# Performance work log

Hardware: AMD Instinct MI355X
Metric: run time of the kernel (lower is better)

## Reference

```python
import math
import jax, jax.numpy as jnp
import numpy as np

B_SZ, N_TOK, D_INNER, S_STATE = 4, 1024, 384, 16
DT_MAX = 0.15


def setup_inputs() -> dict:
    key = jax.random.key(0)
    ks = jax.random.split(key, 10)
    dt_init = math.log(math.exp(0.1) - 1.0)  # softplus^-1(0.1)
    x = jax.random.normal(ks[0], (B_SZ, N_TOK, D_INNER), dtype=jnp.float32)
    dt_self_W = jax.random.uniform(ks[1], (D_INNER, D_INNER), minval=-1e-4, maxval=1e-4)
    dt_self_b = jnp.full((D_INNER,), dt_init, dtype=jnp.float32)
    dt_diff_W = jax.random.uniform(ks[2], (D_INNER, D_INNER), minval=-1e-4, maxval=1e-4)
    dt_diff_b = jnp.full((D_INNER,), dt_init, dtype=jnp.float32)
    B_W = jax.random.normal(ks[3], (D_INNER, S_STATE)) / math.sqrt(D_INNER)
    C_real_W = jax.random.normal(ks[4], (D_INNER, S_STATE)) / math.sqrt(D_INNER)
    C_imag_W = jax.random.normal(ks[5], (D_INNER, S_STATE)) / math.sqrt(D_INNER)
    D_param = jnp.ones((D_INNER,), dtype=jnp.float32)
    A_log = jnp.broadcast_to(jnp.log(jnp.arange(1, S_STATE + 1, dtype=jnp.float32))[None, :], (D_INNER, S_STATE))
    lap = jnp.array([[0.0, 1.0, 0.0], [1.0, -4.0, 1.0], [0.0, 1.0, 0.0]], dtype=jnp.float32) * 0.1
    conv_w = jnp.broadcast_to(lap[None, None], (D_INNER, 1, 3, 3)) + 0.01 * jax.random.normal(ks[6], (D_INNER, 1, 3, 3))
    reaction_alpha = 0.01 * jax.random.normal(ks[7], (1, 1, D_INNER, 1))
    reaction_beta = 0.01 * jax.random.normal(ks[8], (1, 1, D_INNER, 1))
    return {
        'x': x, 'dt_self_W': dt_self_W, 'dt_self_b': dt_self_b,
        'dt_diff_W': dt_diff_W, 'dt_diff_b': dt_diff_b,
        'B_W': B_W, 'C_real_W': C_real_W, 'C_imag_W': C_imag_W,
        'D_param': D_param, 'A_log': A_log, 'conv_w': conv_w,
        'reaction_alpha': reaction_alpha, 'reaction_beta': reaction_beta,
        'K_steps': 2,
    }


def _laplacian(h, conv_w, H, W):
    # h: (B, N, D, S) -> depthwise 3x3 conv with replicate pad over the HxW grid
    B, N, D, S = h.shape
    hs = h.transpose(0, 3, 2, 1).reshape(B * S, D, H, W)
    hp = jnp.pad(hs, ((0, 0), (0, 0), (1, 1), (1, 1)), mode='edge')
    lap = jax.lax.conv_general_dilated(
        hp, conv_w, window_strides=(1, 1), padding='VALID',
        feature_group_count=D, dimension_numbers=('NCHW', 'OIHW', 'NCHW'))
    return lap.reshape(B, S, D, N).transpose(0, 3, 2, 1)


def reference(x, dt_self_W, dt_self_b, dt_diff_W, dt_diff_b, B_W, C_real_W,
              C_imag_W, D_param, A_log, conv_w, reaction_alpha, reaction_beta,
              K_steps):
    B, N, D = x.shape
    H = Wg = int(math.sqrt(N))
    A = -jax.nn.softplus(A_log)  # (D, S)
    delta_s = jnp.minimum(jax.nn.softplus(x @ dt_self_W.T + dt_self_b), DT_MAX)[..., None]
    delta_d = jnp.minimum(jax.nn.softplus(x @ dt_diff_W.T + dt_diff_b), DT_MAX)[..., None]
    B_mat = x @ B_W          # (B, N, S)
    C_real = x @ C_real_W    # (B, N, S)
    C_imag = x @ C_imag_W    # (B, N, S)
    mamba_input = jnp.einsum('bnd,bns->bnds', x, B_mat)
    h_real = mamba_input
    h_imag = jnp.zeros_like(h_real)
    dt = 1.0 / K_steps
    A_exp = A[None, None]  # (1,1,D,S)
    for _ in range(K_steps):
        f1_real = delta_s * (A_exp * h_real + mamba_input)
        f1_imag = delta_s * (A_exp * h_imag)
        lap_real = _laplacian(h_real, conv_w, H, Wg)
        lap_imag = _laplacian(h_imag, conv_w, H, Wg)
        f2_real = delta_d * -lap_imag
        f2_imag = delta_d * lap_real
        reaction_scale = reaction_alpha - reaction_beta * (h_real ** 2 + h_imag ** 2)
        h_real = h_real + dt * (f1_real + f2_real + h_real * reaction_scale)
        h_imag = h_imag + dt * (f1_imag + f2_imag + h_imag * reaction_scale)
    y = (jnp.einsum('bnds,bns->bnd', h_real, C_real)
         + jnp.einsum('bnds,bns->bnd', h_imag, C_imag)
         + x * D_param)
    return y
```

## Files before the change

### kernel.cpp

```cpp
#include <hip/hip_runtime.h>
#include <math.h>

#define B_SZ    4
#define N_TOKC  1024
#define D_INNER 384
#define S_STATE 16
#define DT_MAX_V 0.15f
#define PLANE   (B_SZ * N_TOKC)
#define DN      ((size_t)B_SZ * D_INNER * N_TOKC)

typedef __attribute__((ext_vector_type(8))) short bf16x8;
typedef __attribute__((ext_vector_type(4))) float f32x4;

__device__ __forceinline__ float softplusf(float z) {
    return fmaxf(z, 0.f) + log1pf(expf(-fabsf(z)));
}

__device__ __forceinline__ unsigned short f2bf(float f) {
    unsigned u = __float_as_uint(f);
    unsigned r = (u + 0x7FFFu + ((u >> 16) & 1u)) >> 16;
    return (unsigned short)r;
}

__device__ __forceinline__ unsigned packbf(float hr, float hi) {
    return (__float_as_uint(hr) & 0xFFFF0000u) | (__float_as_uint(hi) >> 16);
}

__device__ __forceinline__ size_t frag_off(int T, int kb, int q, int l16) {
    return ((size_t)((T * 12 + kb) * 4 + q)) * 128 + l16 * 8;
}

__device__ __forceinline__ bf16x8 pack8(const float* v) {
    bf16x8 o;
#pragma unroll
    for (int e = 0; e < 8; e++) o[e] = (short)f2bf(v[e]);
    return o;
}

__global__ __launch_bounds__(256) void k_prep(
    const float* __restrict__ x, const float* __restrict__ Ws, const float* __restrict__ Wd,
    const float* __restrict__ BW, const float* __restrict__ CrW, const float* __restrict__ CiW,
    float* __restrict__ x_t, unsigned short* __restrict__ xp,
    unsigned short* __restrict__ Wdtp, unsigned short* __restrict__ Wbcp)
{
    const int t = threadIdx.x;
    const int bx = blockIdx.x;
    if (bx < 1536) {
        __shared__ __align__(16) float tile[32][36];
        const int tok0 = (bx & 127) * 32;
        const int d0   = (bx >> 7) * 32;
        const int b = tok0 >> 10, n0 = tok0 & 1023;
        {
            const int r = t >> 3, c4 = (t & 7) * 4;
            const float4 v = *(const float4*)(x + (size_t)(tok0 + r) * D_INNER + d0 + c4);
            tile[r][c4 + 0] = v.x; tile[r][c4 + 1] = v.y;
            tile[r][c4 + 2] = v.z; tile[r][c4 + 3] = v.w;
        }
        __syncthreads();
        {
            const int dr = t >> 3, n4 = (t & 7) * 4;
            float4 o;
            o.x = tile[n4 + 0][dr]; o.y = tile[n4 + 1][dr];
            o.z = tile[n4 + 2][dr]; o.w = tile[n4 + 3][dr];
            *(float4*)(x_t + ((size_t)(b * D_INNER + d0 + dr)) * N_TOKC + n0 + n4) = o;
        }
        if (t < 128) {
            const int tt = t >> 6, q = (t >> 4) & 3, l16 = t & 15;
            const int row = tt * 16 + l16;
            float v[8];
#pragma unroll
            for (int e = 0; e < 8; e++) v[e] = tile[row][q * 8 + e];
            *(bf16x8*)(xp + frag_off((tok0 >> 4) + tt, d0 >> 5, q, l16)) = pack8(v);
        }
    } else if (bx < 1584) {
        const int vv = bx - 1536;
        const int mat = vv >= 24;
        const int dt16 = mat ? vv - 24 : vv;
        const float* W = mat ? Wd : Ws;
        unsigned short* dst = Wdtp + (size_t)mat * 147456;
#pragma unroll
        for (int it = 0; it < 3; it++) {
            const int item = t + it * 256;
            const int l16 = item & 15, q = (item >> 4) & 3, kb = item >> 6;
            const float* src = W + (size_t)(dt16 * 16 + l16) * D_INNER + kb * 32 + q * 8;
            float v[8];
            const float4 v0 = *(const float4*)(src);
            const float4 v1 = *(const float4*)(src + 4);
            v[0] = v0.x; v[1] = v0.y; v[2] = v0.z; v[3] = v0.w;
            v[4] = v1.x; v[5] = v1.y; v[6] = v1.z; v[7] = v1.w;
            *(bf16x8*)(dst + frag_off(dt16, kb, q, l16)) = pack8(v);
        }
    } else {
        const int m = bx - 1584;
        const float* W2 = (m == 0) ? BW : ((m == 1) ? CrW : CiW);
#pragma unroll
        for (int it = 0; it < 3; it++) {
            const int item = t + it * 256;
            const int l16 = item & 15, q = (item >> 4) & 3, kb = item >> 6;
            float v[8];
#pragma unroll
            for (int e = 0; e < 8; e++)
                v[e] = W2[(size_t)(kb * 32 + q * 8 + e) * S_STATE + l16];
            *(bf16x8*)(Wbcp + (size_t)m * 6144 + frag_off(0, kb, q, l16)) = pack8(v);
        }
    }
}

__global__ __launch_bounds__(256) void k_gemm(
    const unsigned short* __restrict__ xp, const unsigned short* __restrict__ Wdtp,
    const unsigned short* __restrict__ Wbcp,
    const float* __restrict__ bs, const float* __restrict__ bd,
    float* __restrict__ ds_t, float* __restrict__ dd_t,
    float* __restrict__ Bm_t, float* __restrict__ Cr_t, float* __restrict__ Ci_t)
{
    const int wave = threadIdx.x >> 6;
    const int lane = threadIdx.x & 63;
    const int quad = lane >> 4, l16 = lane & 15;

    if (blockIdx.x < 384) {
        const int dbase = (blockIdx.x >> 6) * 64;
        const int tbase = (blockIdx.x & 63) * 64;
        const int wd = (wave & 1) * 32;
        const int wt = (wave >> 1) * 32;
        const int dT0 = (dbase + wd) >> 4;
        const int tT0 = (tbase + wt) >> 4;

        f32x4 acc[2][2][2];
#pragma unroll
        for (int m = 0; m < 2; m++)
#pragma unroll
            for (int i = 0; i < 2; i++)
#pragma unroll
                for (int j = 0; j < 2; j++) acc[m][i][j] = (f32x4)0.f;

#pragma unroll
        for (int kb = 0; kb < 12; kb++) {
            bf16x8 a[2][2], b[2];
#pragma unroll
            for (int m = 0; m < 2; m++)
#pragma unroll
                for (int i = 0; i < 2; i++)
                    a[m][i] = *(const bf16x8*)(Wdtp + (size_t)m * 147456
                                               + frag_off(dT0 + i, kb, quad, l16));
#pragma unroll
            for (int j = 0; j < 2; j++)
                b[j] = *(const bf16x8*)(xp + frag_off(tT0 + j, kb, quad, l16));
#pragma unroll
            for (int m = 0; m < 2; m++)
#pragma unroll
                for (int i = 0; i < 2; i++)
#pragma unroll
                    for (int j = 0; j < 2; j++)
                        acc[m][i][j] = __builtin_amdgcn_mfma_f32_16x16x32_bf16(
                            a[m][i], b[j], acc[m][i][j], 0, 0, 0);
        }

#pragma unroll
        for (int m = 0; m < 2; m++) {
            const float* bias = (m == 0) ? bs : bd;
            float* out = (m == 0) ? ds_t : dd_t;
#pragma unroll
            for (int i = 0; i < 2; i++)
#pragma unroll
                for (int j = 0; j < 2; j++) {
                    const int tok = tbase + wt + j * 16 + l16;
                    const int bb = tok >> 10, n = tok & 1023;
#pragma unroll
                    for (int reg = 0; reg < 4; reg++) {
                        const int d = dbase + wd + i * 16 + quad * 4 + reg;
                        const float v = fminf(softplusf(acc[m][i][j][reg] + bias[d]), DT_MAX_V);
                        out[((size_t)(bb * D_INNER + d)) * N_TOKC + n] = v;
                    }
                }
        }
    } else {
        const int tT = (blockIdx.x - 384) * 4 + wave;
        f32x4 acc[3];
#pragma unroll
        for (int m = 0; m < 3; m++) acc[m] = (f32x4)0.f;

#pragma unroll
        for (int kb = 0; kb < 12; kb++) {
            const bf16x8 b = *(const bf16x8*)(xp + frag_off(tT, kb, quad, l16));
#pragma unroll
            for (int m = 0; m < 3; m++) {
                const bf16x8 a = *(const bf16x8*)(Wbcp + (size_t)m * 6144
                                                  + frag_off(0, kb, quad, l16));
                acc[m] = __builtin_amdgcn_mfma_f32_16x16x32_bf16(a, b, acc[m], 0, 0, 0);
            }
        }

        const int tok = tT * 16 + l16;
#pragma unroll
        for (int m = 0; m < 3; m++) {
            float* plane = (m == 0) ? Bm_t : ((m == 1) ? Cr_t : Ci_t);
#pragma unroll
            for (int reg = 0; reg < 4; reg++) {
                const int s = quad * 4 + reg;
                plane[(size_t)s * PLANE + tok] = acc[m][reg];
            }
        }
    }
}

__global__ __launch_bounds__(256) void k_ssm(
    const float* __restrict__ x_t, const float* __restrict__ conv_w, const float* __restrict__ A_log,
    const float* __restrict__ ralpha, const float* __restrict__ rbeta, const float* __restrict__ Dp,
    const float* __restrict__ ds_t, const float* __restrict__ dd_t,
    const float* __restrict__ Bm_t, const float* __restrict__ Cr_t, const float* __restrict__ Ci_t,
    float* __restrict__ y_part)
{
    const int sg = blockIdx.x;
    const int d  = blockIdx.y;
    const int b  = blockIdx.z;
    const int t  = threadIdx.x;
    const int c  = t & 31;
    const int g  = t >> 5;
    const int r0 = g * 4;

    __shared__ unsigned pl[4][34 * 34];

    float w[9];
#pragma unroll
    for (int i = 0; i < 9; i++) w[i] = conv_w[d * 9 + i];
    const float alpha = ralpha[d];
    const float beta  = rbeta[d];
    const float Dv    = Dp[d];
    float A[4];
#pragma unroll
    for (int s = 0; s < 4; s++) A[s] = -softplusf(A_log[d * S_STATE + sg * 4 + s]);

    const size_t base_dn = ((size_t)(b * D_INNER + d)) * N_TOKC;
    const size_t base_sn = (size_t)b * N_TOKC;

    float xv[4], dsv[4], ddv[4], Bmv[4][4];
    float hr[4][4], hi[4][4];
#pragma unroll
    for (int k = 0; k < 4; k++) {
        const int n = (r0 + k) * 32 + c;
        xv[k]  = x_t [base_dn + n];
        dsv[k] = ds_t[base_dn + n];
        ddv[k] = dd_t[base_dn + n];
#pragma unroll
        for (int s = 0; s < 4; s++) {
            Bmv[k][s] = Bm_t[(size_t)(sg * 4 + s) * PLANE + base_sn + n];
            hr[k][s]  = xv[k] * Bmv[k][s];
        }
    }

    const int wslot = (r0 + 1) * 34 + (c + 1);
    const int rbase = r0 * 34 + c;

#pragma unroll
    for (int s = 0; s < 4; s++) {
#pragma unroll
        for (int k = 0; k < 4; k++)
            pl[s][wslot + k * 34] = __float_as_uint(hr[k][s]);
        if (g == 0) pl[s][c + 1]           = __float_as_uint(hr[0][s]);
        if (g == 7) pl[s][33 * 34 + c + 1] = __float_as_uint(hr[3][s]);
        if (c == 0) {
#pragma unroll
            for (int k = 0; k < 4; k++) pl[s][(r0 + 1 + k) * 34] = __float_as_uint(hr[k][s]);
            if (g == 0) pl[s][0]       = __float_as_uint(hr[0][s]);
            if (g == 7) pl[s][33 * 34] = __float_as_uint(hr[3][s]);
        }
        if (c == 31) {
#pragma unroll
            for (int k = 0; k < 4; k++) pl[s][(r0 + 1 + k) * 34 + 33] = __float_as_uint(hr[k][s]);
            if (g == 0) pl[s][33]           = __float_as_uint(hr[0][s]);
            if (g == 7) pl[s][33 * 34 + 33] = __float_as_uint(hr[3][s]);
        }
    }
    __syncthreads();

    float lr0[4][4];
#pragma unroll
    for (int s = 0; s < 4; s++) {
        float fr[6][3];
#pragma unroll
        for (int rr = 0; rr < 6; rr++)
#pragma unroll
            for (int bb = 0; bb < 3; bb++)
                fr[rr][bb] = __uint_as_float(pl[s][rbase + rr * 34 + bb]);
#pragma unroll
        for (int k = 0; k < 4; k++) {
            float ar = 0.f;
#pragma unroll
            for (int a = 0; a < 3; a++)
#pragma unroll
                for (int bb = 0; bb < 3; bb++)
                    ar = fmaf(w[a * 3 + bb], fr[k + a][bb], ar);
            lr0[k][s] = ar;
        }
    }
    __syncthreads();

#pragma unroll
    for (int k = 0; k < 4; k++)
#pragma unroll
        for (int s = 0; s < 4; s++) {
            const float hrv = hr[k][s];
            const float u   = xv[k] * Bmv[k][s];
            const float f1r = dsv[k] * fmaf(A[s], hrv, u);
            const float rs  = fmaf(-beta, hrv * hrv, alpha);
            hr[k][s] = hrv + 0.5f * (f1r + hrv * rs);
            hi[k][s] = 0.5f * ddv[k] * lr0[k][s];
        }

#pragma unroll
    for (int s = 0; s < 4; s++) {
#pragma unroll
        for (int k = 0; k < 4; k++)
            pl[s][wslot + k * 34] = packbf(hr[k][s], hi[k][s]);
        if (g == 0) pl[s][c + 1]           = packbf(hr[0][s], hi[0][s]);
        if (g == 7) pl[s][33 * 34 + c + 1] = packbf(hr[3][s], hi[3][s]);
        if (c == 0) {
#pragma unroll
            for (int k = 0; k < 4; k++) pl[s][(r0 + 1 + k) * 34] = packbf(hr[k][s], hi[k][s]);
            if (g == 0) pl[s][0]       = packbf(hr[0][s], hi[0][s]);
            if (g == 7) pl[s][33 * 34] = packbf(hr[3][s], hi[3][s]);
        }
        if (c == 31) {
#pragma unroll
            for (int k = 0; k < 4; k++) pl[s][(r0 + 1 + k) * 34 + 33] = packbf(hr[k][s], hi[k][s]);
            if (g == 0) pl[s][33]           = packbf(hr[0][s], hi[0][s]);
            if (g == 7) pl[s][33 * 34 + 33] = packbf(hr[3][s], hi[3][s]);
        }
    }
    __syncthreads();

    float lr1[4][4], li1[4][4];
#pragma unroll
    for (int s = 0; s < 4; s++) {
        float fr[6][3], fi[6][3];
#pragma unroll
        for (int rr = 0; rr < 6; rr++)
#pragma unroll
            for (int bb = 0; bb < 3; bb++) {
                const unsigned u = pl[s][rbase + rr * 34 + bb];
                fr[rr][bb] = __uint_as_float(u & 0xFFFF0000u);
                fi[rr][bb] = __uint_as_float(u << 16);
            }
#pragma unroll
        for (int k = 0; k < 4; k++) {
            float ar = 0.f, ai = 0.f;
#pragma unroll
            for (int a = 0; a < 3; a++)
#pragma unroll
                for (int bb = 0; bb < 3; bb++) {
                    const float wt = w[a * 3 + bb];
                    ar = fmaf(wt, fr[k + a][bb], ar);
                    ai = fmaf(wt, fi[k + a][bb], ai);
                }
            lr1[k][s] = ar; li1[k][s] = ai;
        }
    }

#pragma unroll
    for (int k = 0; k < 4; k++)
#pragma unroll
        for (int s = 0; s < 4; s++) {
            const float hrv = hr[k][s], hiv = hi[k][s];
            const float u   = xv[k] * Bmv[k][s];
            const float f1r = dsv[k] * fmaf(A[s], hrv, u);
            const float f1i = dsv[k] * (A[s] * hiv);
            const float f2r = -ddv[k] * li1[k][s];
            const float f2i =  ddv[k] * lr1[k][s];
            const float q   = fmaf(hrv, hrv, hiv * hiv);
            const float rs  = fmaf(-beta, q, alpha);
            hr[k][s] = hrv + 0.5f * (f1r + f2r + hrv * rs);
            hi[k][s] = hiv + 0.5f * (f1i + f2i + hiv * rs);
        }

#pragma unroll
    for (int k = 0; k < 4; k++) {
        const int n = (r0 + k) * 32 + c;
        float yp = 0.f;
#pragma unroll
        for (int s = 0; s < 4; s++) {
            const size_t po = (size_t)(sg * 4 + s) * PLANE + base_sn + n;
            yp = fmaf(hr[k][s], Cr_t[po], yp);
            yp = fmaf(hi[k][s], Ci_t[po], yp);
        }
        if (sg == 0) yp = fmaf(xv[k], Dv, yp);
        y_part[((size_t)((sg * B_SZ + b) * D_INNER + d)) * N_TOKC + n] = yp;
    }
}

__global__ __launch_bounds__(256) void k_reduce(
    const float* __restrict__ y_part, float* __restrict__ y)
{
    const int d0 = blockIdx.x * 32;
    const int n0 = blockIdx.y * 32;
    const int b  = blockIdx.z;
    const int t  = threadIdx.x;
    __shared__ __align__(16) float tile[32][36];

    const int dr = t >> 3, nc4 = (t & 7) * 4;
    float4 acc = make_float4(0.f, 0.f, 0.f, 0.f);
#pragma unroll
    for (int sg = 0; sg < 4; sg++) {
        const float4 v = *(const float4*)(y_part
            + ((size_t)((sg * B_SZ + b) * D_INNER + d0 + dr)) * N_TOKC + n0 + nc4);
        acc.x += v.x; acc.y += v.y; acc.z += v.z; acc.w += v.w;
    }
    *(float4*)&tile[dr][nc4] = acc;
    __syncthreads();

    const int nr = t >> 3, dc4 = (t & 7) * 4;
    float4 o;
    o.x = tile[dc4 + 0][nr];
    o.y = tile[dc4 + 1][nr];
    o.z = tile[dc4 + 2][nr];
    o.w = tile[dc4 + 3][nr];
    *(float4*)(y + ((size_t)(b * N_TOKC + n0 + nr)) * D_INNER + d0 + dc4) = o;
}

extern "C" void kernel_launch(void* const* d_in, const int* in_sizes, int n_in,
                              void* d_out, int out_size, void* d_ws, size_t ws_size,
                              hipStream_t stream)
{
    const float* x    = (const float*)d_in[0];
    const float* Ws   = (const float*)d_in[1];
    const float* bsb  = (const float*)d_in[2];
    const float* Wd   = (const float*)d_in[3];
    const float* bdb  = (const float*)d_in[4];
    const float* BW   = (const float*)d_in[5];
    const float* CrW  = (const float*)d_in[6];
    const float* CiW  = (const float*)d_in[7];
    const float* Dp   = (const float*)d_in[8];
    const float* Alog = (const float*)d_in[9];
    const float* cw   = (const float*)d_in[10];
    const float* ra   = (const float*)d_in[11];
    const float* rb   = (const float*)d_in[12];
    float* y = (float*)d_out;

    float* ws     = (float*)d_ws;
    float* ds_t   = ws;
    float* dd_t   = ds_t + DN;
    float* x_t    = dd_t + DN;
    float* Bm_t   = x_t + DN;
    float* Cr_t   = Bm_t + (size_t)S_STATE * PLANE;
    float* Ci_t   = Cr_t + (size_t)S_STATE * PLANE;
    float* y_part = Ci_t + (size_t)S_STATE * PLANE;

    unsigned short* xp   = (unsigned short*)y_part;
    unsigned short* Wdtp = xp + (size_t)256 * 12 * 4 * 128;
    unsigned short* Wbcp = Wdtp + (size_t)2 * 147456;

    k_prep<<<dim3(1587), 256, 0, stream>>>(x, Ws, Wd, BW, CrW, CiW, x_t, xp, Wdtp, Wbcp);
    k_gemm<<<dim3(448), 256, 0, stream>>>(xp, Wdtp, Wbcp, bsb, bdb,
                                          ds_t, dd_t, Bm_t, Cr_t, Ci_t);
    k_ssm<<<dim3(4, D_INNER, B_SZ), 256, 0, stream>>>(x_t, cw, Alog, ra, rb, Dp,
                                                      ds_t, dd_t, Bm_t, Cr_t, Ci_t, y_part);
    k_reduce<<<dim3(12, 32, 4), 256, 0, stream>>>(y_part, y);
}
```

Before: 175.9 us.

## Fuse prep and GEMM into one front kernel with on-the-fly bf16 conversion

Removes the separate packing kernel: the dt GEMM now reads fp32 x and weights directly and truncates them to bf16 fragments in registers, while the B/C projection blocks compute in fp32 through shared-memory tiles and also write the transposed x_t. This drops one launch and the round trip through packed bf16 buffers. In exchange the dt GEMM does strided fp32 global loads with redundant reads across blocks, and the conversion now truncates instead of rounding to nearest. The SSM update is also reorganised with pre-halved coefficients and fewer multiplies.

```diff
diff --git a/kernel.cpp b/kernel.cpp
--- a/kernel.cpp
+++ b/kernel.cpp
@@ -16,114 +16,40 @@
     return fmaxf(z, 0.f) + log1pf(expf(-fabsf(z)));
 }
 
-__device__ __forceinline__ unsigned short f2bf(float f) {
-    unsigned u = __float_as_uint(f);
-    unsigned r = (u + 0x7FFFu + ((u >> 16) & 1u)) >> 16;
-    return (unsigned short)r;
-}
-
 __device__ __forceinline__ unsigned packbf(float hr, float hi) {
     return (__float_as_uint(hr) & 0xFFFF0000u) | (__float_as_uint(hi) >> 16);
 }
 
-__device__ __forceinline__ size_t frag_off(int T, int kb, int q, int l16) {
-    return ((size_t)((T * 12 + kb) * 4 + q)) * 128 + l16 * 8;
-}
-
-__device__ __forceinline__ bf16x8 pack8(const float* v) {
-    bf16x8 o;
-#pragma unroll
-    for (int e = 0; e < 8; e++) o[e] = (short)f2bf(v[e]);
-    return o;
-}
-
-__global__ __launch_bounds__(256) void k_prep(
+__device__ __forceinline__ bf16x8 load_frag_f32(const float* __restrict__ p) {
+    const float4 v0 = *(const float4*)p;
+    const float4 v1 = *(const float4*)(p + 4);
+    union { bf16x8 v; unsigned w[4]; } o;
+    o.w[0] = (__float_as_uint(v0.y) & 0xFFFF0000u) | (__float_as_uint(v0.x) >> 16);
+    o.w[1] = (__float_as_uint(v0.w) & 0xFFFF0000u) | (__float_as_uint(v0.z) >> 16);
+    o.w[2] = (__float_as_uint(v1.y) & 0xFFFF0000u) | (__float_as_uint(v1.x) >> 16);
+    o.w[3] = (__float_as_uint(v1.w) & 0xFFFF0000u) | (__float_as_uint(v1.z) >> 16);
+    return o.v;
+}
+
+__global__ __launch_bounds__(256) void k_front(
     const float* __restrict__ x, const float* __restrict__ Ws, const float* __restrict__ Wd,
+    const float* __restrict__ bs, const float* __restrict__ bd,
     const float* __restrict__ BW, const float* __restrict__ CrW, const float* __restrict__ CiW,
-    float* __restrict__ x_t, unsigned short* __restrict__ xp,
-    unsigned short* __restrict__ Wdtp, unsigned short* __restrict__ Wbcp)
-{
-    const int t = threadIdx.x;
-    const int bx = blockIdx.x;
-    if (bx < 1536) {
-        __shared__ __align__(16) float tile[32][36];
-        const int tok0 = (bx & 127) * 32;
-        const int d0   = (bx >> 7) * 32;
-        const int b = tok0 >> 10, n0 = tok0 & 1023;
-        {
-            const int r = t >> 3, c4 = (t & 7) * 4;
-            const float4 v = *(const float4*)(x + (size_t)(tok0 + r) * D_INNER + d0 + c4);
-            tile[r][c4 + 0] = v.x; tile[r][c4 + 1] = v.y;
-            tile[r][c4 + 2] = v.z; tile[r][c4 + 3] = v.w;
-        }
-        __syncthreads();
-        {
-            const int dr = t >> 3, n4 = (t & 7) * 4;
-            float4 o;
-            o.x = tile[n4 + 0][dr]; o.y = tile[n4 + 1][dr];
-            o.z = tile[n4 + 2][dr]; o.w = tile[n4 + 3][dr];
-            *(float4*)(x_t + ((size_t)(b * D_INNER + d0 + dr)) * N_TOKC + n0 + n4) = o;
-        }
-        if (t < 128) {
-            const int tt = t >> 6, q = (t >> 4) & 3, l16 = t & 15;
-            const int row = tt * 16 + l16;
-            float v[8];
-#pragma unroll
-            for (int e = 0; e < 8; e++) v[e] = tile[row][q * 8 + e];
-            *(bf16x8*)(xp + frag_off((tok0 >> 4) + tt, d0 >> 5, q, l16)) = pack8(v);
-        }
-    } else if (bx < 1584) {
-        const int vv = bx - 1536;
-        const int mat = vv >= 24;
-        const int dt16 = mat ? vv - 24 : vv;
-        const float* W = mat ? Wd : Ws;
-        unsigned short* dst = Wdtp + (size_t)mat * 147456;
-#pragma unroll
-        for (int it = 0; it < 3; it++) {
-            const int item = t + it * 256;
-            const int l16 = item & 15, q = (item >> 4) & 3, kb = item >> 6;
-            const float* src = W + (size_t)(dt16 * 16 + l16) * D_INNER + kb * 32 + q * 8;
-            float v[8];
-            const float4 v0 = *(const float4*)(src);
-            const float4 v1 = *(const float4*)(src + 4);
-            v[0] = v0.x; v[1] = v0.y; v[2] = v0.z; v[3] = v0.w;
-            v[4] = v1.x; v[5] = v1.y; v[6] = v1.z; v[7] = v1.w;
-            *(bf16x8*)(dst + frag_off(dt16, kb, q, l16)) = pack8(v);
-        }
-    } else {
-        const int m = bx - 1584;
-        const float* W2 = (m == 0) ? BW : ((m == 1) ? CrW : CiW);
-#pragma unroll
-        for (int it = 0; it < 3; it++) {
-            const int item = t + it * 256;
-            const int l16 = item & 15, q = (item >> 4) & 3, kb = item >> 6;
-            float v[8];
-#pragma unroll
-            for (int e = 0; e < 8; e++)
-                v[e] = W2[(size_t)(kb * 32 + q * 8 + e) * S_STATE + l16];
-            *(bf16x8*)(Wbcp + (size_t)m * 6144 + frag_off(0, kb, q, l16)) = pack8(v);
-        }
-    }
-}
-
-__global__ __launch_bounds__(256) void k_gemm(
-    const unsigned short* __restrict__ xp, const unsigned short* __restrict__ Wdtp,
-    const unsigned short* __restrict__ Wbcp,
-    const float* __restrict__ bs, const float* __restrict__ bd,
-    float* __restrict__ ds_t, float* __restrict__ dd_t,
+    float* __restrict__ ds_t, float* __restrict__ dd_t, float* __restrict__ x_t,
     float* __restrict__ Bm_t, float* __restrict__ Cr_t, float* __restrict__ Ci_t)
 {
-    const int wave = threadIdx.x >> 6;
-    const int lane = threadIdx.x & 63;
-    const int quad = lane >> 4, l16 = lane & 15;
+    __shared__ __align__(16) float xs[16][68];
+    __shared__ __align__(16) float wsv[16][52];
+
+    const int t = threadIdx.x;
 
     if (blockIdx.x < 384) {
+        const int wave = t >> 6, lane = t & 63;
+        const int quad = lane >> 4, l16 = lane & 15;
         const int dbase = (blockIdx.x >> 6) * 64;
         const int tbase = (blockIdx.x & 63) * 64;
         const int wd = (wave & 1) * 32;
         const int wt = (wave >> 1) * 32;
-        const int dT0 = (dbase + wd) >> 4;
-        const int tT0 = (tbase + wt) >> 4;
 
         f32x4 acc[2][2][2];
 #pragma unroll
@@ -135,16 +61,17 @@
 
 #pragma unroll
         for (int kb = 0; kb < 12; kb++) {
+            const int kf = kb * 32 + quad * 8;
             bf16x8 a[2][2], b[2];
 #pragma unroll
-            for (int m = 0; m < 2; m++)
-#pragma unroll
-                for (int i = 0; i < 2; i++)
-                    a[m][i] = *(const bf16x8*)(Wdtp + (size_t)m * 147456
-                                               + frag_off(dT0 + i, kb, quad, l16));
+            for (int i = 0; i < 2; i++) {
+                const int row = dbase + wd + i * 16 + l16;
+                a[0][i] = load_frag_f32(Ws + (size_t)row * D_INNER + kf);
+                a[1][i] = load_frag_f32(Wd + (size_t)row * D_INNER + kf);
+            }
 #pragma unroll
             for (int j = 0; j < 2; j++)
-                b[j] = *(const bf16x8*)(xp + frag_off(tT0 + j, kb, quad, l16));
+                b[j] = load_frag_f32(x + (size_t)(tbase + wt + j * 16 + l16) * D_INNER + kf);
 #pragma unroll
             for (int m = 0; m < 2; m++)
 #pragma unroll
@@ -174,31 +101,59 @@
                 }
         }
     } else {
-        const int tT = (blockIdx.x - 384) * 4 + wave;
-        f32x4 acc[3];
-#pragma unroll
-        for (int m = 0; m < 3; m++) acc[m] = (f32x4)0.f;
-
-#pragma unroll
-        for (int kb = 0; kb < 12; kb++) {
-            const bf16x8 b = *(const bf16x8*)(xp + frag_off(tT, kb, quad, l16));
-#pragma unroll
-            for (int m = 0; m < 3; m++) {
-                const bf16x8 a = *(const bf16x8*)(Wbcp + (size_t)m * 6144
-                                                  + frag_off(0, kb, quad, l16));
-                acc[m] = __builtin_amdgcn_mfma_f32_16x16x32_bf16(a, b, acc[m], 0, 0, 0);
-            }
-        }
-
-        const int tok = tT * 16 + l16;
-#pragma unroll
-        for (int m = 0; m < 3; m++) {
-            float* plane = (m == 0) ? Bm_t : ((m == 1) ? Cr_t : Ci_t);
-#pragma unroll
-            for (int reg = 0; reg < 4; reg++) {
-                const int s = quad * 4 + reg;
-                plane[(size_t)s * PLANE + tok] = acc[m][reg];
-            }
+        const int tok0 = (blockIdx.x - 384) * 64;
+        const int bb = tok0 >> 10, n0 = tok0 & 1023;
+        const int tm = t & 15;
+        const int tn = t >> 4;
+
+        float acc[4][3];
+#pragma unroll
+        for (int i = 0; i < 4; i++)
+#pragma unroll
+            for (int c = 0; c < 3; c++) acc[i][c] = 0.f;
+
+        for (int k0 = 0; k0 < D_INNER; k0 += 16) {
+            {
+                const int m = t >> 2, k4 = (t & 3) * 4;
+                const float4 v = *(const float4*)(x + (size_t)(tok0 + m) * D_INNER + k0 + k4);
+                xs[k4 + 0][m] = v.x; xs[k4 + 1][m] = v.y; xs[k4 + 2][m] = v.z; xs[k4 + 3][m] = v.w;
+            }
+            {
+                const int kk = t >> 4, s = t & 15;
+                wsv[kk][s]      = BW [(size_t)(k0 + kk) * S_STATE + s];
+                wsv[kk][16 + s] = CrW[(size_t)(k0 + kk) * S_STATE + s];
+                wsv[kk][32 + s] = CiW[(size_t)(k0 + kk) * S_STATE + s];
+            }
+            __syncthreads();
+
+            {
+                const int kk = t >> 4, m4 = (t & 15) * 4;
+                const float4 v = *(const float4*)&xs[kk][m4];
+                *(float4*)(x_t + ((size_t)(bb * D_INNER + k0 + kk)) * N_TOKC + n0 + m4) = v;
+            }
+
+#pragma unroll
+            for (int kk = 0; kk < 16; kk++) {
+                const float4 a = *(const float4*)&xs[kk][4 * tm];
+                const float av[4] = { a.x, a.y, a.z, a.w };
+#pragma unroll
+                for (int c = 0; c < 3; c++) {
+                    const float bv = wsv[kk][3 * tn + c];
+#pragma unroll
+                    for (int i = 0; i < 4; i++) acc[i][c] = fmaf(av[i], bv, acc[i][c]);
+                }
+            }
+            __syncthreads();
+        }
+
+#pragma unroll
+        for (int c = 0; c < 3; c++) {
+            const int col = 3 * tn + c;
+            const int mat = col >> 4, s = col & 15;
+            float* plane = (mat == 0) ? Bm_t : ((mat == 1) ? Cr_t : Ci_t);
+#pragma unroll
+            for (int i = 0; i < 4; i++)
+                plane[(size_t)s * PLANE + tok0 + 4 * tm + i] = acc[i][c];
         }
     }
 }
@@ -223,9 +178,9 @@
     float w[9];
 #pragma unroll
     for (int i = 0; i < 9; i++) w[i] = conv_w[d * 9 + i];
-    const float alpha = ralpha[d];
-    const float beta  = rbeta[d];
-    const float Dv    = Dp[d];
+    const float alpha2 = 0.5f * ralpha[d];
+    const float beta2  = 0.5f * rbeta[d];
+    const float Dv     = Dp[d];
     float A[4];
 #pragma unroll
     for (int s = 0; s < 4; s++) A[s] = -softplusf(A_log[d * S_STATE + sg * 4 + s]);
@@ -233,18 +188,18 @@
     const size_t base_dn = ((size_t)(b * D_INNER + d)) * N_TOKC;
     const size_t base_sn = (size_t)b * N_TOKC;
 
-    float xv[4], dsv[4], ddv[4], Bmv[4][4];
+    float xv[4], ds2[4], dd2[4], u[4][4];
     float hr[4][4], hi[4][4];
 #pragma unroll
     for (int k = 0; k < 4; k++) {
         const int n = (r0 + k) * 32 + c;
         xv[k]  = x_t [base_dn + n];
-        dsv[k] = ds_t[base_dn + n];
-        ddv[k] = dd_t[base_dn + n];
+        ds2[k] = 0.5f * ds_t[base_dn + n];
+        dd2[k] = 0.5f * dd_t[base_dn + n];
 #pragma unroll
         for (int s = 0; s < 4; s++) {
-            Bmv[k][s] = Bm_t[(size_t)(sg * 4 + s) * PLANE + base_sn + n];
-            hr[k][s]  = xv[k] * Bmv[k][s];
+            u[k][s]  = xv[k] * Bm_t[(size_t)(sg * 4 + s) * PLANE + base_sn + n];
+            hr[k][s] = u[k][s];
         }
     }
 
@@ -300,11 +255,12 @@
 #pragma unroll
         for (int s = 0; s < 4; s++) {
             const float hrv = hr[k][s];
-            const float u   = xv[k] * Bmv[k][s];
-            const float f1r = dsv[k] * fmaf(A[s], hrv, u);
-            const float rs  = fmaf(-beta, hrv * hrv, alpha);
-            hr[k][s] = hrv + 0.5f * (f1r + hrv * rs);
-            hi[k][s] = 0.5f * ddv[k] * lr0[k][s];
+            const float tt  = fmaf(A[s], hrv, u[k][s]);
+            const float rs2 = fmaf(-beta2, hrv * hrv, alpha2);
+            float S = ds2[k] * tt;
+            S = fmaf(hrv, rs2, S);
+            hr[k][s] = hrv + S;
+            hi[k][s] = dd2[k] * lr0[k][s];
         }
 
 #pragma unroll
@@ -337,9 +293,9 @@
         for (int rr = 0; rr < 6; rr++)
 #pragma unroll
             for (int bb = 0; bb < 3; bb++) {
-                const unsigned u = pl[s][rbase + rr * 34 + bb];
-                fr[rr][bb] = __uint_as_float(u & 0xFFFF0000u);
-                fi[rr][bb] = __uint_as_float(u << 16);
+                const unsigned uu = pl[s][rbase + rr * 34 + bb];
+                fr[rr][bb] = __uint_as_float(uu & 0xFFFF0000u);
+                fi[rr][bb] = __uint_as_float(uu << 16);
             }
 #pragma unroll
         for (int k = 0; k < 4; k++) {
@@ -361,15 +317,18 @@
 #pragma unroll
         for (int s = 0; s < 4; s++) {
             const float hrv = hr[k][s], hiv = hi[k][s];
-            const float u   = xv[k] * Bmv[k][s];
-            const float f1r = dsv[k] * fmaf(A[s], hrv, u);
-            const float f1i = dsv[k] * (A[s] * hiv);
-            const float f2r = -ddv[k] * li1[k][s];
-            const float f2i =  ddv[k] * lr1[k][s];
             const float q   = fmaf(hrv, hrv, hiv * hiv);
-            const float rs  = fmaf(-beta, q, alpha);
-            hr[k][s] = hrv + 0.5f * (f1r + f2r + hrv * rs);
-            hi[k][s] = hiv + 0.5f * (f1i + f2i + hiv * rs);
+            const float rs2 = fmaf(-beta2, q, alpha2);
+            const float tr  = fmaf(A[s], hrv, u[k][s]);
+            float Sr = ds2[k] * tr;
+            Sr = fmaf(-dd2[k], li1[k][s], Sr);
+            Sr = fmaf(hrv, rs2, Sr);
+            const float ti = A[s] * hiv;
+            float Si = ds2[k] * ti;
+            Si = fmaf(dd2[k], lr1[k][s], Si);
+            Si = fmaf(hiv, rs2, Si);
+            hr[k][s] = hrv + Sr;
+            hi[k][s] = hiv + Si;
         }
 
 #pragma unroll
@@ -444,13 +403,8 @@
     float* Ci_t   = Cr_t + (size_t)S_STATE * PLANE;
     float* y_part = Ci_t + (size_t)S_STATE * PLANE;
 
-    unsigned short* xp   = (unsigned short*)y_part;
-    unsigned short* Wdtp = xp + (size_t)256 * 12 * 4 * 128;
-    unsigned short* Wbcp = Wdtp + (size_t)2 * 147456;
-
-    k_prep<<<dim3(1587), 256, 0, stream>>>(x, Ws, Wd, BW, CrW, CiW, x_t, xp, Wdtp, Wbcp);
-    k_gemm<<<dim3(448), 256, 0, stream>>>(xp, Wdtp, Wbcp, bsb, bdb,
-                                          ds_t, dd_t, Bm_t, Cr_t, Ci_t);
+    k_front<<<dim3(448), 256, 0, stream>>>(x, Ws, Wd, bsb, bdb, BW, CrW, CiW,
+                                           ds_t, dd_t, x_t, Bm_t, Cr_t, Ci_t);
     k_ssm<<<dim3(4, D_INNER, B_SZ), 256, 0, stream>>>(x_t, cw, Alog, ra, rb, Dp,
                                                       ds_t, dd_t, Bm_t, Cr_t, Ci_t, y_part);
     k_reduce<<<dim3(12, 32, 4), 256, 0, stream>>>(y_part, y);
```

New measurement: 199.5 us. 1.13x slower.
